# Optimization experiments

Measured on AMD Instinct MI355X. Metric: run time of the kernel, lower is better.

The kernel has to match this reference:

```python
import jax, jax.numpy as jnp
import numpy as np

L, B, E = 128, 16, 512
C_OUT = 64
KERNELS = [1, 3, 5, 7]
M = len(KERNELS) * C_OUT          # mlpdec_in = 256
OUT_SIZE = 256
SLOPE = 0.1


def setup_inputs() -> dict:
    key = jax.random.key(0)
    ks = jax.random.split(key, 32)
    s = 0.02
    d = {"x": jax.random.normal(ks[0], (L, B, E), dtype=jnp.float32)}
    # conv branches: weight (C_out, 1, k, E), bias (C_out,)
    for i, k in enumerate(KERNELS):
        d[f"cw{i}"] = jax.random.normal(ks[1 + 2 * i], (C_OUT, 1, k, E), dtype=jnp.float32) * s
        d[f"cb{i}"] = jnp.zeros((C_OUT,), dtype=jnp.float32)
    dims = [(C_OUT, 2 * M), (C_OUT, C_OUT), (C_OUT, C_OUT), (C_OUT, C_OUT)]
    for i, (o, inn) in enumerate(dims):
        d[f"mw{i}"] = jax.random.normal(ks[10 + 2 * i], (o, inn), dtype=jnp.float32) * s
        d[f"mb{i}"] = jnp.zeros((o,), dtype=jnp.float32)
    # mlp_layer: Linear(C->C), Linear(C->output_size)
    d["lw0"] = jax.random.normal(ks[20], (C_OUT, C_OUT), dtype=jnp.float32) * s
    d["lb0"] = jnp.zeros((C_OUT,), dtype=jnp.float32)
    d["lw1"] = jax.random.normal(ks[21], (OUT_SIZE, C_OUT), dtype=jnp.float32) * s
    d["lb1"] = jnp.zeros((OUT_SIZE,), dtype=jnp.float32)
    return d


def _lrelu(x):
    return jax.nn.leaky_relu(x, SLOPE)


def _conv_branch(xb, w, b):
    # xb: (B,1,L,E), w: (C,1,k,E) -> (B,C,L)
    k = w.shape[2]
    pad = (k - 1) // 2
    y = jax.lax.conv_general_dilated(
        xb, w, window_strides=(1, 1), padding=[(pad, pad), (0, 0)],
        dimension_numbers=("NCHW", "OIHW", "NCHW"))
    return _lrelu(y[..., 0] + b[None, :, None])


def reference(x, cw0, cb0, cw1, cb1, cw2, cb2, cw3, cb3,
              mw0, mb0, mw1, mb1, mw2, mb2, mw3, mb3,
              lw0, lb0, lw1, lb1):
    # x: (L,B,E) -> (B,1,L,E)
    xb = jnp.transpose(x, (1, 0, 2))[:, None, :, :]
    feats = jnp.concatenate([
        _conv_branch(xb, cw0, cb0), _conv_branch(xb, cw1, cb1),
        _conv_branch(xb, cw2, cb2), _conv_branch(xb, cw3, cb3)], axis=1)  # (B, 4C, L)
    f = jnp.transpose(feats, (2, 0, 1))  # (L, B, M)
    # pairwise: pair[i, j] = [f[j], f[i]]  -> (L, L, B, 2M)
    a = jnp.broadcast_to(f[None, :, :, :], (L, L, B, M))
    bpart = jnp.broadcast_to(f[:, None, :, :], (L, L, B, M))
    h = jnp.concatenate([a, bpart], axis=-1)
    for w, bb in ((mw0, mb0), (mw1, mb1), (mw2, mb2), (mw3, mb3)):
        h = _lrelu(h @ w.T + bb)
    h = h.sum(axis=0)  # (L, B, C)
    h = _lrelu(h @ lw0.T + lb0)
    return _lrelu(h @ lw1.T + lb1)  # (L, B, OUT_SIZE)
```

## Files before the change

### kernel.cpp

```cpp
#include <hip/hip_runtime.h>
#include <hip/hip_bf16.h>

#define SLOPE 0.1f
typedef unsigned short u16;
typedef unsigned int u32;
typedef __attribute__((ext_vector_type(8))) short short8;
typedef __attribute__((ext_vector_type(4))) float floatx4;

__device__ __forceinline__ float lrelu(float x) { return x > 0.0f ? x : SLOPE * x; }

__device__ __forceinline__ void split_rn(float x, u16* h, u16* l) {
    union { __hip_bfloat16 b; u16 u; } c1, c2;
    c1.b = __float2bfloat16(x);
    float hf = __bfloat162float(c1.b);
    c2.b = __float2bfloat16(x - hf);
    *h = c1.u; *l = c2.u;
}

__device__ __forceinline__ void pack2x2(float v0, float v1, u32& h, u32& l) {
    u32 a0 = __float_as_uint(v0), a1 = __float_as_uint(v1);
    h = __builtin_amdgcn_perm(a1, a0, 0x07060302u);
    float r0 = v0 - __uint_as_float(a0 & 0xFFFF0000u);
    float r1 = v1 - __uint_as_float(a1 & 0xFFFF0000u);
    l = __builtin_amdgcn_perm(__float_as_uint(r1), __float_as_uint(r0), 0x07060302u);
}

__device__ __forceinline__ short8 load_frag(const u16* p) {
    union { uint4 q; short8 s; } cv;
    cv.q = *(const uint4*)p;
    return cv.s;
}

__device__ __forceinline__ floatx4 mfma16(short8 a, short8 b, floatx4 c) {
    return __builtin_amdgcn_mfma_f32_16x16x32_bf16(a, b, c, 0, 0, 0);
}

__global__ __launch_bounds__(256) void p0_prep(
    const float* __restrict__ x,
    const float* __restrict__ cw0, const float* __restrict__ cw1,
    const float* __restrict__ cw2, const float* __restrict__ cw3,
    const float* __restrict__ mw0, const float* __restrict__ mw1,
    const float* __restrict__ mw2, const float* __restrict__ mw3,
    const float* __restrict__ lw0, const float* __restrict__ lw1,
    u16* __restrict__ xfh, u16* __restrict__ xfl,
    u16* __restrict__ wcfh, u16* __restrict__ wcfl,
    u16* __restrict__ b2fh, u16* __restrict__ b2fl,
    u16* __restrict__ w3fh, u16* __restrict__ w3fl,
    float* __restrict__ lw0t, float* __restrict__ lw1t)
{
    int idx = blockIdx.x * 256 + threadIdx.x;
    if (idx < 1048576) {
        const int j = idx & 7, lane = (idx >> 3) & 63;
        const int kc = (idx >> 9) & 15, rt = idx >> 13;
        const int l15 = lane & 15, quad = lane >> 4;
        split_rn(x[(rt * 16 + l15) * 512 + kc * 32 + quad * 8 + j], &xfh[idx], &xfl[idx]);
        return;
    }
    idx -= 1048576;
    if (idx < 524288) {
        const int j = idx & 7, lane = (idx >> 3) & 63;
        const int kc = (idx >> 9) & 15, nt = (idx >> 13) & 3, slot = idx >> 15;
        int branch, base;
        if (slot == 0)      { branch = 0; base = 0; }
        else if (slot < 4)  { branch = 1; base = 1; }
        else if (slot < 9)  { branch = 2; base = 4; }
        else                { branch = 3; base = 9; }
        const int dk = slot - base, ksz = 2 * branch + 1;
        const float* cw = branch == 0 ? cw0 : branch == 1 ? cw1 : branch == 2 ? cw2 : cw3;
        const int c = nt * 16 + (lane & 15);
        const int e = kc * 32 + (lane >> 4) * 8 + j;
        split_rn(cw[(c * ksz + dk) * 512 + e], &wcfh[idx], &wcfl[idx]);
        return;
    }
    idx -= 524288;
    if (idx < 32768) {
        const int j = idx & 7, lane = (idx >> 3) & 63;
        const int kc = (idx >> 9) & 7, nt = (idx >> 12) & 3, nh = idx >> 14;
        const int n = nh * 64 + nt * 16 + (lane & 15);
        const int k = kc * 32 + (lane >> 4) * 8 + j;
        split_rn(mw0[(n & 63) * 512 + (n >> 6) * 256 + k], &b2fh[idx], &b2fl[idx]);
        return;
    }
    idx -= 32768;
    if (idx < 12288) {
        const int j = idx & 7, lane = (idx >> 3) & 63;
        const int kc = (idx >> 9) & 1, mt = (idx >> 10) & 3, layer = idx >> 12;
        const float* mw = layer == 0 ? mw1 : layer == 1 ? mw2 : mw3;
        const int ch = mt * 16 + (lane & 15);
        const int k = kc * 32 + (lane >> 4) * 8 + j;
        split_rn(mw[ch * 64 + k], &w3fh[idx], &w3fl[idx]);
        return;
    }
    idx -= 12288;
    if (idx < 4096) { const int k = idx >> 6, n = idx & 63; lw0t[idx] = lw0[n * 64 + k]; return; }
    idx -= 4096;
    if (idx < 16384) { const int k = idx >> 8, n = idx & 255; lw1t[idx] = lw1[n * 64 + k]; return; }
}

__global__ __launch_bounds__(256) void k1f_conv(
    const u16* __restrict__ xfh, const u16* __restrict__ xfl,
    const u16* __restrict__ wcfh, const u16* __restrict__ wcfl,
    const float* __restrict__ cb0, const float* __restrict__ cb1,
    const float* __restrict__ cb2, const float* __restrict__ cb3,
    u16* __restrict__ Ffh, u16* __restrict__ Ffl)
{
    __shared__ float P[4][16][72];

    const int t = threadIdx.x, lane = t & 63, w = t >> 6;
    const int rt = blockIdx.x;
    const int br = blockIdx.y;
    const int base = br * br;
    const int ksz = 2 * br + 1;
    const int l15 = lane & 15, quad = lane >> 4;

    floatx4 acc[4];
    #pragma unroll
    for (int j = 0; j < 4; ++j) acc[j] = (floatx4)0.0f;

    const int nunits = ksz * 16;
    for (int unit = w; unit < nunits; unit += 4) {
        const int dk = unit >> 4, kc = unit & 15;
        const int rts = rt + dk - br;
        if (rts < 0 || rts >= 128) continue;
        const int aoff = ((rts * 16 + kc) * 64 + lane) * 8;
        const short8 ah = load_frag(xfh + aoff);
        const short8 al = load_frag(xfl + aoff);
        const int slot = base + dk;
        #pragma unroll
        for (int nt = 0; nt < 4; ++nt) {
            const int boff = (((slot * 4 + nt) * 16 + kc) * 64 + lane) * 8;
            const short8 bh = load_frag(wcfh + boff);
            const short8 bl = load_frag(wcfl + boff);
            acc[nt] = mfma16(ah, bh, acc[nt]);
            acc[nt] = mfma16(ah, bl, acc[nt]);
            acc[nt] = mfma16(al, bh, acc[nt]);
        }
    }

    #pragma unroll
    for (int nt = 0; nt < 4; ++nt)
        #pragma unroll
        for (int r = 0; r < 4; ++r)
            P[w][quad * 4 + r][nt * 16 + l15] = acc[nt][r];
    __syncthreads();

    const float* cb = br == 0 ? cb0 : br == 1 ? cb1 : br == 2 ? cb2 : cb3;
    const int row = t >> 4, c4 = (t & 15) * 4;
    u16 h4[4], l4[4];
    #pragma unroll
    for (int i = 0; i < 4; ++i) {
        float val = P[0][row][c4 + i] + P[1][row][c4 + i]
                  + P[2][row][c4 + i] + P[3][row][c4 + i] + cb[c4 + i];
        split_rn(lrelu(val), &h4[i], &l4[i]);
    }
    const int m4 = br * 64 + c4;
    const int dst = ((rt * 8 + (m4 >> 5)) * 64 + ((m4 >> 3) & 3) * 16 + row) * 8 + (m4 & 7);
    *(ushort4*)(Ffh + dst) = make_ushort4(h4[0], h4[1], h4[2], h4[3]);
    *(ushort4*)(Ffl + dst) = make_ushort4(l4[0], l4[1], l4[2], l4[3]);
}

__global__ __launch_bounds__(256) void k2_uv(
    const u16* __restrict__ Ffh, const u16* __restrict__ Ffl,
    const u16* __restrict__ b2fh, const u16* __restrict__ b2fl,
    const float* __restrict__ mb0,
    float* __restrict__ u, float* __restrict__ v_t)
{
    __shared__ float P[4][16][72];

    const int t = threadIdx.x, lane = t & 63, w = t >> 6;
    const int rt = blockIdx.x;
    const int nh = w >> 1, kg = w & 1;
    const int l15 = lane & 15, quad = lane >> 4;

    floatx4 acc[4];
    #pragma unroll
    for (int j = 0; j < 4; ++j) acc[j] = (floatx4)0.0f;

    #pragma unroll
    for (int kk = 0; kk < 4; ++kk) {
        const int kc = kg * 4 + kk;
        const int aoff = ((rt * 8 + kc) * 64 + lane) * 8;
        const short8 ah = load_frag(Ffh + aoff);
        const short8 al = load_frag(Ffl + aoff);
        #pragma unroll
        for (int nt = 0; nt < 4; ++nt) {
            const int boff = (((nh * 4 + nt) * 8 + kc) * 64 + lane) * 8;
            const short8 bh = load_frag(b2fh + boff);
            const short8 bl = load_frag(b2fl + boff);
            acc[nt] = mfma16(ah, bh, acc[nt]);
            acc[nt] = mfma16(ah, bl, acc[nt]);
            acc[nt] = mfma16(al, bh, acc[nt]);
        }
    }

    #pragma unroll
    for (int nt = 0; nt < 4; ++nt)
        #pragma unroll
        for (int r = 0; r < 4; ++r)
            P[w][quad * 4 + r][nt * 16 + l15] = acc[nt][r];
    __syncthreads();

    const int row = t >> 4, c4 = (t & 15) * 4;
    const int rglob = rt * 16 + row;
    const int i = rglob >> 4, b = rglob & 15;
    float4 uu, vv;
    uu.x = P[0][row][c4 + 0] + P[1][row][c4 + 0] + mb0[c4 + 0];
    uu.y = P[0][row][c4 + 1] + P[1][row][c4 + 1] + mb0[c4 + 1];
    uu.z = P[0][row][c4 + 2] + P[1][row][c4 + 2] + mb0[c4 + 2];
    uu.w = P[0][row][c4 + 3] + P[1][row][c4 + 3] + mb0[c4 + 3];
    vv.x = P[2][row][c4 + 0] + P[3][row][c4 + 0];
    vv.y = P[2][row][c4 + 1] + P[3][row][c4 + 1];
    vv.z = P[2][row][c4 + 2] + P[3][row][c4 + 2];
    vv.w = P[2][row][c4 + 3] + P[3][row][c4 + 3];
    *(float4*)(u + rglob * 64 + c4) = uu;
    *(float4*)(v_t + (b * 128 + i) * 64 + c4) = vv;
}

__global__ __launch_bounds__(128, 2) void k3_pair(
    const float* __restrict__ u, const float* __restrict__ v_t,
    const u16* __restrict__ w3fh, const u16* __restrict__ w3fl,
    const float* __restrict__ mb1, const float* __restrict__ mb2,
    const float* __restrict__ mb3,
    float* __restrict__ Spart)
{
    __shared__ __align__(16) u16 Hh[128][72];
    __shared__ __align__(16) u16 Hl[128][72];
    __shared__ __align__(16) float us[64];

    const int t = threadIdx.x, lane = t & 63, w = t >> 6;
    const int jb = blockIdx.x, b = jb & 15;
    const int l15 = lane & 15, quad = lane >> 4;
    const int i0 = w * 64;

    if (t < 64) us[t] = u[jb * 64 + t];
    __syncthreads();

    const float* vb = v_t + (b * 128 + i0) * 64;
    #pragma unroll
    for (int n = 0; n < 16; ++n) {
        const int idx = n * 64 + lane;
        const int il = idx >> 4, c4 = (idx & 15) * 4;
        const float4 vv = *(const float4*)(vb + idx * 4);
        const float4 uu = *(const float4*)(&us[c4]);
        const float a0 = lrelu(vv.x + uu.x), a1 = lrelu(vv.y + uu.y);
        const float a2 = lrelu(vv.z + uu.z), a3 = lrelu(vv.w + uu.w);
        u32 h01, l01, h23, l23;
        pack2x2(a0, a1, h01, l01);
        pack2x2(a2, a3, h23, l23);
        *(uint2*)&Hh[i0 + il][c4] = make_uint2(h01, h23);
        *(uint2*)&Hl[i0 + il][c4] = make_uint2(l01, l23);
    }

    const float* mbp[3] = {mb1, mb2, mb3};
    for (int layer = 0; layer < 3; ++layer) {
        floatx4 acc[4][4];
        #pragma unroll
        for (int i = 0; i < 4; ++i)
            #pragma unroll
            for (int j = 0; j < 4; ++j) acc[i][j] = (floatx4)0.0f;

        #pragma unroll
        for (int kc = 0; kc < 2; ++kc) {
            short8 ah[4], al[4];
            #pragma unroll
            for (int mt = 0; mt < 4; ++mt) {
                const int aoff = (((layer * 4 + mt) * 2 + kc) * 64 + lane) * 8;
                ah[mt] = load_frag(w3fh + aoff);
                al[mt] = load_frag(w3fl + aoff);
            }
            const int k0 = kc * 32 + quad * 8;
            #pragma unroll
            for (int nt = 0; nt < 4; ++nt) {
                const short8 bh = load_frag(&Hh[i0 + nt * 16 + l15][k0]);
                const short8 bl = load_frag(&Hl[i0 + nt * 16 + l15][k0]);
                #pragma unroll
                for (int mt = 0; mt < 4; ++mt) {
                    acc[mt][nt] = mfma16(ah[mt], bh, acc[mt][nt]);
                    acc[mt][nt] = mfma16(ah[mt], bl, acc[mt][nt]);
                    acc[mt][nt] = mfma16(al[mt], bh, acc[mt][nt]);
                }
            }
        }

        if (layer < 2) {
            #pragma unroll
            for (int mt = 0; mt < 4; ++mt) {
                float bias[4];
                #pragma unroll
                for (int r = 0; r < 4; ++r) bias[r] = mbp[layer][mt * 16 + quad * 4 + r];
                #pragma unroll
                for (int nt = 0; nt < 4; ++nt) {
                    const int i = i0 + nt * 16 + l15;
                    const float v0 = lrelu(acc[mt][nt][0] + bias[0]);
                    const float v1 = lrelu(acc[mt][nt][1] + bias[1]);
                    const float v2 = lrelu(acc[mt][nt][2] + bias[2]);
                    const float v3 = lrelu(acc[mt][nt][3] + bias[3]);
                    u32 h01, l01, h23, l23;
                    pack2x2(v0, v1, h01, l01);
                    pack2x2(v2, v3, h23, l23);
                    *(uint2*)&Hh[i][mt * 16 + quad * 4] = make_uint2(h01, h23);
                    *(uint2*)&Hl[i][mt * 16 + quad * 4] = make_uint2(l01, l23);
                }
            }
        } else {
            #pragma unroll
            for (int mt = 0; mt < 4; ++mt) {
                float bias[4];
                #pragma unroll
                for (int r = 0; r < 4; ++r) bias[r] = mbp[2][mt * 16 + quad * 4 + r];
                float4 sv;
                #pragma unroll
                for (int r = 0; r < 4; ++r) {
                    float val = lrelu(acc[mt][0][r] + bias[r])
                              + lrelu(acc[mt][1][r] + bias[r])
                              + lrelu(acc[mt][2][r] + bias[r])
                              + lrelu(acc[mt][3][r] + bias[r]);
                    val += __shfl_xor(val, 1, 16);
                    val += __shfl_xor(val, 2, 16);
                    val += __shfl_xor(val, 4, 16);
                    val += __shfl_xor(val, 8, 16);
                    (&sv.x)[r] = val;
                }
                if (l15 == 0)
                    *(float4*)(Spart + jb * 128 + w * 64 + mt * 16 + quad * 4) = sv;
            }
        }
    }
}

__global__ __launch_bounds__(256) void k4_head(
    const float* __restrict__ Spart,
    const float* __restrict__ lw0t, const float* __restrict__ lb0,
    const float* __restrict__ lw1t, const float* __restrict__ lb1,
    float* __restrict__ out)
{
    __shared__ float Ss[8][64];
    __shared__ float T1[8][64];

    const int t = threadIdx.x;
    const int jb0 = blockIdx.x * 8;

    #pragma unroll
    for (int p = 0; p < 2; ++p) {
        const int idx = t + 256 * p;
        const int jbb = idx >> 6, ch = idx & 63;
        Ss[jbb][ch] = Spart[(jb0 + jbb) * 128 + ch] + Spart[(jb0 + jbb) * 128 + 64 + ch];
    }
    __syncthreads();

    #pragma unroll
    for (int p = 0; p < 2; ++p) {
        const int idx = t + 256 * p;
        const int jbb = idx >> 6, c = idx & 63;
        float a = lb0[c];
        #pragma unroll 8
        for (int k = 0; k < 64; ++k) a += Ss[jbb][k] * lw0t[k * 64 + c];
        T1[jbb][c] = lrelu(a);
    }
    __syncthreads();

    const int c = t;
    float acc[8];
    const float base = lb1[c];
    #pragma unroll
    for (int jbb = 0; jbb < 8; ++jbb) acc[jbb] = base;
    #pragma unroll 4
    for (int k = 0; k < 64; ++k) {
        const float wv = lw1t[k * 256 + c];
        #pragma unroll
        for (int jbb = 0; jbb < 8; ++jbb) acc[jbb] += T1[jbb][k] * wv;
    }
    #pragma unroll
    for (int jbb = 0; jbb < 8; ++jbb)
        out[(jb0 + jbb) * 256 + c] = lrelu(acc[jbb]);
}

extern "C" void kernel_launch(void* const* d_in, const int* in_sizes, int n_in,
                              void* d_out, int out_size, void* d_ws, size_t ws_size,
                              hipStream_t stream)
{
    const float* x   = (const float*)d_in[0];
    const float* cw0 = (const float*)d_in[1];
    const float* cb0 = (const float*)d_in[2];
    const float* cw1 = (const float*)d_in[3];
    const float* cb1 = (const float*)d_in[4];
    const float* cw2 = (const float*)d_in[5];
    const float* cb2 = (const float*)d_in[6];
    const float* cw3 = (const float*)d_in[7];
    const float* cb3 = (const float*)d_in[8];
    const float* mw0 = (const float*)d_in[9];
    const float* mb0 = (const float*)d_in[10];
    const float* mw1 = (const float*)d_in[11];
    const float* mb1 = (const float*)d_in[12];
    const float* mw2 = (const float*)d_in[13];
    const float* mb2 = (const float*)d_in[14];
    const float* mw3 = (const float*)d_in[15];
    const float* mb3 = (const float*)d_in[16];
    const float* lw0 = (const float*)d_in[17];
    const float* lb0 = (const float*)d_in[18];
    const float* lw1 = (const float*)d_in[19];
    const float* lb1 = (const float*)d_in[20];
    float* out = (float*)d_out;

    char* base = (char*)d_ws;
    u16* xfh   = (u16*)(base + 0);
    u16* xfl   = (u16*)(base + 2097152);
    u16* wcfh  = (u16*)(base + 4194304);
    u16* wcfl  = (u16*)(base + 5242880);
    u16* b2fh  = (u16*)(base + 6291456);
    u16* b2fl  = (u16*)(base + 6356992);
    u16* w3fh  = (u16*)(base + 6422528);
    u16* w3fl  = (u16*)(base + 6447104);
    float* lw0t  = (float*)(base + 6471680);
    float* lw1t  = (float*)(base + 6488064);
    u16* Ffh   = (u16*)(base + 6553600);
    u16* Ffl   = (u16*)(base + 7602176);
    float* u   = (float*)(base + 8650752);
    float* v_t = (float*)(base + 9175040);
    float* Spart = (float*)(base + 9699328);

    hipLaunchKernelGGL(p0_prep, dim3(6400), dim3(256), 0, stream,
                       x, cw0, cw1, cw2, cw3, mw0, mw1, mw2, mw3, lw0, lw1,
                       xfh, xfl, wcfh, wcfl, b2fh, b2fl, w3fh, w3fl, lw0t, lw1t);
    hipLaunchKernelGGL(k1f_conv, dim3(128, 4), dim3(256), 0, stream,
                       xfh, xfl, wcfh, wcfl, cb0, cb1, cb2, cb3, Ffh, Ffl);
    hipLaunchKernelGGL(k2_uv, dim3(128), dim3(256), 0, stream,
                       Ffh, Ffl, b2fh, b2fl, mb0, u, v_t);
    hipLaunchKernelGGL(k3_pair, dim3(2048), dim3(128), 0, stream,
                       u, v_t, w3fh, w3fl, mb1, mb2, mb3, Spart);
    hipLaunchKernelGGL(k4_head, dim3(256), dim3(256), 0, stream,
                       Spart, lw0t, lb0, lw1t, lb1, out);
}
```

Measured before the change: 185.8 us.

## Split k2 over output halves and widen k3 to four waves per block

k2_uv gains a second grid dimension so each block computes either u or v, with its four waves splitting the K dimension, doubling the block count. k3_pair now runs four waves of 32 pair rows each instead of two waves of 64, which halves accumulator registers per wave and raises the occupancy hint to 4. Spart grows to four partials per row, and k4_head sums all four. The aim is more parallelism and latency hiding in the dominant pair kernel, at the cost of reloading the weight fragments in twice as many waves.

```diff
diff --git a/kernel.cpp b/kernel.cpp
--- a/kernel.cpp
+++ b/kernel.cpp
@@ -169,7 +169,7 @@
 
     const int t = threadIdx.x, lane = t & 63, w = t >> 6;
     const int rt = blockIdx.x;
-    const int nh = w >> 1, kg = w & 1;
+    const int nh = blockIdx.y;
     const int l15 = lane & 15, quad = lane >> 4;
 
     floatx4 acc[4];
@@ -177,8 +177,8 @@
     for (int j = 0; j < 4; ++j) acc[j] = (floatx4)0.0f;
 
     #pragma unroll
-    for (int kk = 0; kk < 4; ++kk) {
-        const int kc = kg * 4 + kk;
+    for (int kk = 0; kk < 2; ++kk) {
+        const int kc = w * 2 + kk;
         const int aoff = ((rt * 8 + kc) * 64 + lane) * 8;
         const short8 ah = load_frag(Ffh + aoff);
         const short8 al = load_frag(Ffl + aoff);
@@ -202,21 +202,22 @@
 
     const int row = t >> 4, c4 = (t & 15) * 4;
     const int rglob = rt * 16 + row;
-    const int i = rglob >> 4, b = rglob & 15;
-    float4 uu, vv;
-    uu.x = P[0][row][c4 + 0] + P[1][row][c4 + 0] + mb0[c4 + 0];
-    uu.y = P[0][row][c4 + 1] + P[1][row][c4 + 1] + mb0[c4 + 1];
-    uu.z = P[0][row][c4 + 2] + P[1][row][c4 + 2] + mb0[c4 + 2];
-    uu.w = P[0][row][c4 + 3] + P[1][row][c4 + 3] + mb0[c4 + 3];
-    vv.x = P[2][row][c4 + 0] + P[3][row][c4 + 0];
-    vv.y = P[2][row][c4 + 1] + P[3][row][c4 + 1];
-    vv.z = P[2][row][c4 + 2] + P[3][row][c4 + 2];
-    vv.w = P[2][row][c4 + 3] + P[3][row][c4 + 3];
-    *(float4*)(u + rglob * 64 + c4) = uu;
-    *(float4*)(v_t + (b * 128 + i) * 64 + c4) = vv;
-}
-
-__global__ __launch_bounds__(128, 2) void k3_pair(
+    float4 oo;
+    #pragma unroll
+    for (int i = 0; i < 4; ++i)
+        (&oo.x)[i] = P[0][row][c4 + i] + P[1][row][c4 + i]
+                   + P[2][row][c4 + i] + P[3][row][c4 + i];
+    if (nh == 0) {
+        oo.x += mb0[c4 + 0]; oo.y += mb0[c4 + 1];
+        oo.z += mb0[c4 + 2]; oo.w += mb0[c4 + 3];
+        *(float4*)(u + rglob * 64 + c4) = oo;
+    } else {
+        const int i = rglob >> 4, b = rglob & 15;
+        *(float4*)(v_t + (b * 128 + i) * 64 + c4) = oo;
+    }
+}
+
+__global__ __launch_bounds__(256, 4) void k3_pair(
     const float* __restrict__ u, const float* __restrict__ v_t,
     const u16* __restrict__ w3fh, const u16* __restrict__ w3fl,
     const float* __restrict__ mb1, const float* __restrict__ mb2,
@@ -230,14 +231,14 @@
     const int t = threadIdx.x, lane = t & 63, w = t >> 6;
     const int jb = blockIdx.x, b = jb & 15;
     const int l15 = lane & 15, quad = lane >> 4;
-    const int i0 = w * 64;
+    const int i0 = w * 32;
 
     if (t < 64) us[t] = u[jb * 64 + t];
     __syncthreads();
 
     const float* vb = v_t + (b * 128 + i0) * 64;
     #pragma unroll
-    for (int n = 0; n < 16; ++n) {
+    for (int n = 0; n < 8; ++n) {
         const int idx = n * 64 + lane;
         const int il = idx >> 4, c4 = (idx & 15) * 4;
         const float4 vv = *(const float4*)(vb + idx * 4);
@@ -253,11 +254,11 @@
 
     const float* mbp[3] = {mb1, mb2, mb3};
     for (int layer = 0; layer < 3; ++layer) {
-        floatx4 acc[4][4];
+        floatx4 acc[4][2];
         #pragma unroll
         for (int i = 0; i < 4; ++i)
             #pragma unroll
-            for (int j = 0; j < 4; ++j) acc[i][j] = (floatx4)0.0f;
+            for (int j = 0; j < 2; ++j) acc[i][j] = (floatx4)0.0f;
 
         #pragma unroll
         for (int kc = 0; kc < 2; ++kc) {
@@ -270,7 +271,7 @@
             }
             const int k0 = kc * 32 + quad * 8;
             #pragma unroll
-            for (int nt = 0; nt < 4; ++nt) {
+            for (int nt = 0; nt < 2; ++nt) {
                 const short8 bh = load_frag(&Hh[i0 + nt * 16 + l15][k0]);
                 const short8 bl = load_frag(&Hl[i0 + nt * 16 + l15][k0]);
                 #pragma unroll
@@ -289,7 +290,7 @@
                 #pragma unroll
                 for (int r = 0; r < 4; ++r) bias[r] = mbp[layer][mt * 16 + quad * 4 + r];
                 #pragma unroll
-                for (int nt = 0; nt < 4; ++nt) {
+                for (int nt = 0; nt < 2; ++nt) {
                     const int i = i0 + nt * 16 + l15;
                     const float v0 = lrelu(acc[mt][nt][0] + bias[0]);
                     const float v1 = lrelu(acc[mt][nt][1] + bias[1]);
@@ -312,9 +313,7 @@
                 #pragma unroll
                 for (int r = 0; r < 4; ++r) {
                     float val = lrelu(acc[mt][0][r] + bias[r])
-                              + lrelu(acc[mt][1][r] + bias[r])
-                              + lrelu(acc[mt][2][r] + bias[r])
-                              + lrelu(acc[mt][3][r] + bias[r]);
+                              + lrelu(acc[mt][1][r] + bias[r]);
                     val += __shfl_xor(val, 1, 16);
                     val += __shfl_xor(val, 2, 16);
                     val += __shfl_xor(val, 4, 16);
@@ -322,7 +321,7 @@
                     (&sv.x)[r] = val;
                 }
                 if (l15 == 0)
-                    *(float4*)(Spart + jb * 128 + w * 64 + mt * 16 + quad * 4) = sv;
+                    *(float4*)(Spart + jb * 256 + w * 64 + mt * 16 + quad * 4) = sv;
             }
         }
     }
@@ -344,7 +343,8 @@
     for (int p = 0; p < 2; ++p) {
         const int idx = t + 256 * p;
         const int jbb = idx >> 6, ch = idx & 63;
-        Ss[jbb][ch] = Spart[(jb0 + jbb) * 128 + ch] + Spart[(jb0 + jbb) * 128 + 64 + ch];
+        const float* sp = Spart + (jb0 + jbb) * 256 + ch;
+        Ss[jbb][ch] = sp[0] + sp[64] + sp[128] + sp[192];
     }
     __syncthreads();
 
@@ -424,9 +424,9 @@
                        xfh, xfl, wcfh, wcfl, b2fh, b2fl, w3fh, w3fl, lw0t, lw1t);
     hipLaunchKernelGGL(k1f_conv, dim3(128, 4), dim3(256), 0, stream,
                        xfh, xfl, wcfh, wcfl, cb0, cb1, cb2, cb3, Ffh, Ffl);
-    hipLaunchKernelGGL(k2_uv, dim3(128), dim3(256), 0, stream,
+    hipLaunchKernelGGL(k2_uv, dim3(128, 2), dim3(256), 0, stream,
                        Ffh, Ffl, b2fh, b2fl, mb0, u, v_t);
-    hipLaunchKernelGGL(k3_pair, dim3(2048), dim3(128), 0, stream,
+    hipLaunchKernelGGL(k3_pair, dim3(2048), dim3(256), 0, stream,
                        u, v_t, w3fh, w3fl, mb1, mb2, mb3, Spart);
     hipLaunchKernelGGL(k4_head, dim3(256), dim3(256), 0, stream,
                        Spart, lw0t, lb0, lw1t, lb1, out);
```

Result: faster. 174.8 us (-5.9%).
